# Performance work log

Measured on AMD Instinct MI355X. Metric: run time of the kernel, lower is better.

The kernel has to match this reference:

```python
import jax, jax.numpy as jnp
import numpy as np

N_USER, N_REST, D, E, Q = 200000, 50000, 64, 2000000, 500000


def setup_inputs() -> dict:
    key = jax.random.key(0)
    ks = jax.random.split(key, 16)
    s = 0.05
    return {
        "x_user": jax.random.normal(ks[0], (N_USER, D), jnp.float32),
        "x_rest": jax.random.normal(ks[1], (N_REST, D), jnp.float32),
        "Wl": jax.random.normal(ks[2], (3, 2, D, D), jnp.float32) * s,
        "Wr": jax.random.normal(ks[3], (3, 2, D, D), jnp.float32) * s,
        "bl": jnp.zeros((3, 2, D), jnp.float32),
        "dW1": jax.random.normal(ks[4], (D, 2 * D), jnp.float32) * s,
        "db1": jnp.zeros((D,), jnp.float32),
        "dW2": jax.random.normal(ks[5], (D, D), jnp.float32) * s,
        "db2": jnp.zeros((D,), jnp.float32),
        "dW3": jax.random.normal(ks[6], (1, D), jnp.float32) * s,
        "db3": jnp.zeros((1,), jnp.float32),
        "ur_src": jax.random.randint(ks[7], (E,), 0, N_USER, jnp.int32),
        "ur_dst": jax.random.randint(ks[8], (E,), 0, N_REST, jnp.int32),
        "ru_src": jax.random.randint(ks[9], (E,), 0, N_REST, jnp.int32),
        "ru_dst": jax.random.randint(ks[10], (E,), 0, N_USER, jnp.int32),
        "el_row": jax.random.randint(ks[11], (Q,), 0, N_USER, jnp.int32),
        "el_col": jax.random.randint(ks[12], (Q,), 0, N_REST, jnp.int32),
    }


def _sage(h_src, h_dst, src, dst, W_l, b_l, W_r):
    # PyG SAGEConv: lin_l(mean_{j in N(i)} x_j) + lin_r(x_i); bias on lin_l only.
    n_dst = h_dst.shape[0]
    agg = jax.ops.segment_sum(h_src[src], dst, num_segments=n_dst)  # [n_dst, D]
    cnt = jax.ops.segment_sum(jnp.ones_like(dst, dtype=h_src.dtype), dst, num_segments=n_dst)
    mean = agg / jnp.maximum(cnt, 1)[:, None]
    return mean @ W_l.T + b_l + h_dst @ W_r.T


def reference(x_user, x_rest, Wl, Wr, bl, dW1, db1, dW2, db2, dW3, db3,
              ur_src, ur_dst, ru_src, ru_dst, el_row, el_col):
    hu, hr = x_user, x_rest
    for l in range(3):
        # edge type 0: user -> restaurant ('rates'); edge type 1: reverse
        zr = _sage(hu, hr, ur_src, ur_dst, Wl[l, 0], bl[l, 0], Wr[l, 0])
        zu = _sage(hr, hu, ru_src, ru_dst, Wl[l, 1], bl[l, 1], Wr[l, 1])
        if l < 2:
            zr, zu = jax.nn.relu(zr), jax.nn.relu(zu)
        hu, hr = zu, zr
    # EdgeDecoder
    z = jnp.concatenate([hu[el_row], hr[el_col]], axis=-1)  # [Q, 2D]
    z = jax.nn.relu(z @ dW1.T + db1)
    z = jax.nn.relu(z @ dW2.T + db2)
    z = z @ dW3.T + db3
    return z.reshape(-1)
```

## Files before the change

### kernel.cpp

```cpp
#include <hip/hip_runtime.h>

#define NU 200000
#define NR 50000
#define DD 64
#define NE 2000000
#define NQ 500000
#define NBR 196
#define NBU 782
#define LDW 68

#define NBS 98
#define BKT_CAP 24576
#define LW_U 11
#define LW_R 9
#define PB_E 4096
#define NPBB 489

__global__ __launch_bounds__(256)
void binpass_kernel(const int* __restrict__ ru_src, const int* __restrict__ ru_dst,
                    const int* __restrict__ ur_src, const int* __restrict__ ur_dst,
                    int* __restrict__ bcur, int2* __restrict__ pairs) {
    __shared__ int2 stg[PB_E];
    __shared__ unsigned char gstg[PB_E];
    __shared__ int hist[256];
    __shared__ int sca[256], scb[256];
    __shared__ int gpos[128];
    int side = (blockIdx.x >= NPBB) ? 1 : 0;
    int blk = side ? (blockIdx.x - NPBB) : blockIdx.x;
    const int* src = side ? ur_src : ru_src;
    const int* dst = side ? ur_dst : ru_dst;
    int lw = side ? LW_R : LW_U;
    int* bc = bcur + side * NBS;
    int2* region = pairs + (size_t)side * NBS * BKT_CAP;
    int tid = threadIdx.x;
    hist[tid] = 0;
    __syncthreads();
    int base = blk * PB_E;
    int myg[16]; int myrank[16]; int2 myp[16];
#pragma unroll
    for (int i = 0; i < 16; i++) {
        int e = base + i * 256 + tid;
        if (e < NE) {
            int d = dst[e];
            int g = d >> lw;
            myg[i] = g;
            myp[i] = make_int2(src[e], d);
            myrank[i] = atomicAdd(&hist[g], 1);
        } else myg[i] = -1;
    }
    __syncthreads();
    int h = hist[tid];
    sca[tid] = h;
    __syncthreads();
    int* cur = sca; int* alt = scb;
    for (int off = 1; off < 256; off <<= 1) {
        int x = cur[tid];
        if (tid >= off) x += cur[tid - off];
        alt[tid] = x;
        __syncthreads();
        int* tmp = cur; cur = alt; alt = tmp;
    }
    alt[tid] = cur[tid] - h;
    if (tid < NBS && h > 0) gpos[tid] = atomicAdd(&bc[tid], h);
    __syncthreads();
    int* basep = alt;
#pragma unroll
    for (int i = 0; i < 16; i++) {
        if (myg[i] >= 0) {
            int p = basep[myg[i]] + myrank[i];
            stg[p] = myp[i];
            gstg[p] = (unsigned char)myg[i];
        }
    }
    __syncthreads();
    int tot = cur[255];
    for (int i = tid; i < tot; i += 256) {
        int g = gstg[i];
        int o = g * BKT_CAP + gpos[g] + (i - basep[g]);
        region[o] = stg[i];
    }
}

__global__ void bbase_kernel(const int* __restrict__ bcur, int* __restrict__ bbase,
                             int* __restrict__ rs_u, int* __restrict__ rs_r) {
    __shared__ int a[128], b[128];
    int sidx = blockIdx.x;
    const int* bc = bcur + sidx * NBS;
    int* bb = bbase + sidx * NBS;
    int tid = threadIdx.x;
    a[tid] = (tid < NBS) ? bc[tid] : 0;
    __syncthreads();
    int* cur = a; int* alt = b;
    for (int off = 1; off < 128; off <<= 1) {
        int t = cur[tid];
        if (tid >= off) t += cur[tid - off];
        alt[tid] = t;
        __syncthreads();
        int* tmp = cur; cur = alt; alt = tmp;
    }
    if (tid < NBS) bb[tid] = (tid == 0) ? 0 : cur[tid - 1];
    if (tid == 0) { if (sidx == 0) rs_u[NU] = NE; else rs_r[NR] = NE; }
}

__global__ __launch_bounds__(256)
void fillpass_kernel(const int2* __restrict__ pairs, const int* __restrict__ bcur,
                     const int* __restrict__ bbase,
                     int* __restrict__ rs_u, int* __restrict__ rs_r,
                     int* __restrict__ csr_u, int* __restrict__ csr_r) {
    __shared__ int win[BKT_CAP];
    __shared__ int lcnt[2048];
    __shared__ int lofs[2048];
    __shared__ int tsc[256], tsc2[256];
    int side = (blockIdx.x >= NBS) ? 1 : 0;
    int bkt = side ? (blockIdx.x - NBS) : blockIdx.x;
    const int2* reg = pairs + ((size_t)side * NBS + bkt) * BKT_CAP;
    int* rs = side ? rs_r : rs_u;
    int* csr = side ? csr_r : csr_u;
    int W = side ? 512 : 2048;
    int lw = side ? LW_R : LW_U;
    int n = side ? NR : NU;
    int d0 = bkt << lw;
    int tot = bcur[side * NBS + bkt];
    int base = bbase[side * NBS + bkt];
    int tid = threadIdx.x;
    for (int i = tid; i < W; i += 256) lcnt[i] = 0;
    __syncthreads();
    for (int i = tid; i < tot; i += 256) {
        int2 p = reg[i];
        atomicAdd(&lcnt[p.y - d0], 1);
    }
    __syncthreads();
    int per = W >> 8;
    int b0 = tid * per;
    int run = 0;
    for (int i = 0; i < per; i++) { int v = lcnt[b0 + i]; lofs[b0 + i] = run; run += v; }
    tsc[tid] = run;
    __syncthreads();
    int* cur = tsc; int* alt = tsc2;
    for (int off = 1; off < 256; off <<= 1) {
        int x = cur[tid];
        if (tid >= off) x += cur[tid - off];
        alt[tid] = x;
        __syncthreads();
        int* tmp = cur; cur = alt; alt = tmp;
    }
    int texcl = cur[tid] - run;
    for (int i = 0; i < per; i++) lofs[b0 + i] += texcl;
    __syncthreads();
    int wn = min(W, n - d0);
    for (int i = tid; i < wn; i += 256) rs[d0 + i] = base + lofs[i];
    __syncthreads();
    for (int i = tid; i < tot; i += 256) {
        int2 p = reg[i];
        int slot = atomicAdd(&lofs[p.y - d0], 1);
        win[slot] = p.x;
    }
    __syncthreads();
    for (int i = tid; i < tot; i += 256) csr[base + i] = win[i];
}

__global__ __launch_bounds__(256)
void gather2_kernel(const float* __restrict__ hu, const int* __restrict__ csr_r,
                    const int* __restrict__ rs_r, float* __restrict__ mean_r,
                    const float* __restrict__ hr, const int* __restrict__ csr_u,
                    const int* __restrict__ rs_u, float* __restrict__ mean_u) {
    int lane = threadIdx.x & 63;
    int wave = blockIdx.x * 4 + (threadIdx.x >> 6);
    const float* h; const int* csr; const int* rs; float* mean; int r;
    if (wave < NR) { h = hu; csr = csr_r; rs = rs_r; mean = mean_r; r = wave; }
    else if (wave < NR + NU) { h = hr; csr = csr_u; rs = rs_u; mean = mean_u; r = wave - NR; }
    else return;
    int s = rs[r], e = rs[r + 1];
    int g = lane >> 4;
    int fo = (lane & 15) << 2;
    float4 a0 = {0.f, 0.f, 0.f, 0.f};
    float4 a1 = {0.f, 0.f, 0.f, 0.f};
    for (int j = s; j < e; j += 64) {
        int rem = e - j;
        int nch = rem < 64 ? rem : 64;
        int li = lane < nch ? lane : nch - 1;
        int idx = csr[j + li];
        for (int kk = 0; kk < nch; kk += 8) {
            int j0 = kk + g;
            int j1 = kk + 4 + g;
            int i0 = __shfl(idx, j0);
            int i1 = __shfl(idx, j1);
            float4 x0 = *(const float4*)(h + (size_t)i0 * DD + fo);
            float4 x1 = *(const float4*)(h + (size_t)i1 * DD + fo);
            if (j0 < nch) { a0.x += x0.x; a0.y += x0.y; a0.z += x0.z; a0.w += x0.w; }
            if (j1 < nch) { a1.x += x1.x; a1.y += x1.y; a1.z += x1.z; a1.w += x1.w; }
        }
    }
    float4 acc;
    acc.x = a0.x + a1.x; acc.y = a0.y + a1.y;
    acc.z = a0.z + a1.z; acc.w = a0.w + a1.w;
    acc.x += __shfl_xor(acc.x, 16); acc.y += __shfl_xor(acc.y, 16);
    acc.z += __shfl_xor(acc.z, 16); acc.w += __shfl_xor(acc.w, 16);
    acc.x += __shfl_xor(acc.x, 32); acc.y += __shfl_xor(acc.y, 32);
    acc.z += __shfl_xor(acc.z, 32); acc.w += __shfl_xor(acc.w, 32);
    if (g == 0) {
        float inv = 1.0f / fmaxf((float)(e - s), 1.0f);
        acc.x *= inv; acc.y *= inv; acc.z *= inv; acc.w *= inv;
        *(float4*)(mean + (size_t)r * DD + fo) = acc;
    }
}

#define DOT4(A, B) ((A).x*(B).x + (A).y*(B).y + (A).z*(B).z + (A).w*(B).w)

__global__ __launch_bounds__(256, 2)
void sage_fused_kernel(const float* __restrict__ mean_r, const float* __restrict__ hr,
                       const float* __restrict__ mean_u, const float* __restrict__ hu,
                       const float* __restrict__ Wl2, const float* __restrict__ Wr2,
                       const float* __restrict__ bl2,
                       float* __restrict__ out_r, float* __restrict__ out_u, int do_relu) {
    __shared__ __attribute__((aligned(16))) float Wls[DD * LDW];
    __shared__ __attribute__((aligned(16))) float Wrs[DD * LDW];
    __shared__ __attribute__((aligned(16))) float Ms[64 * LDW];
    __shared__ __attribute__((aligned(16))) float Xs[64 * LDW];
    __shared__ float bsh[DD];
    int side = (blockIdx.x < NBR) ? 0 : 1;
    const float* Wl = Wl2 + side * DD * DD;
    const float* Wr = Wr2 + side * DD * DD;
    const float* bl = bl2 + side * DD;
    const float* mean; const float* h; float* out; int n; int blk;
    if (side == 0) { mean = mean_r; h = hr; out = out_r; n = NR; blk = blockIdx.x; }
    else { mean = mean_u; h = hu; out = out_u; n = NU; blk = blockIdx.x - NBR; }
    int tid = threadIdx.x;
    for (int i = tid; i < DD * DD; i += 256) {
        int c = i >> 6, k = i & 63;
        Wls[c * LDW + k] = Wl[i];
        Wrs[c * LDW + k] = Wr[i];
    }
    if (tid < DD) bsh[tid] = bl[tid];
    int rgrp = tid & 15;
    int cgrp = tid >> 4;
    int cb = cgrp * 4;
    int r00 = blk * 256;
    for (int ch = 0; ch < 4; ch++) {
        int rc0 = r00 + ch * 64;
        __syncthreads();
        for (int i = tid; i < 1024; i += 256) {
            int row = i >> 4;
            int c4 = (i & 15) << 2;
            int gr = min(rc0 + row, n - 1);
            *(float4*)&Ms[row * LDW + c4] = *(const float4*)(mean + (size_t)gr * DD + c4);
            *(float4*)&Xs[row * LDW + c4] = *(const float4*)(h + (size_t)gr * DD + c4);
        }
        __syncthreads();
        float4 bias = {bsh[cb], bsh[cb + 1], bsh[cb + 2], bsh[cb + 3]};
        float4 acc0 = bias, acc1 = bias, acc2 = bias, acc3 = bias;
#pragma unroll 1
        for (int kc = 0; kc < DD; kc += 8) {
            float4 wl[4][2], wr[4][2];
#pragma unroll
            for (int c = 0; c < 4; c++) {
                wl[c][0] = *(const float4*)&Wls[(cb + c) * LDW + kc];
                wl[c][1] = *(const float4*)&Wls[(cb + c) * LDW + kc + 4];
                wr[c][0] = *(const float4*)&Wrs[(cb + c) * LDW + kc];
                wr[c][1] = *(const float4*)&Wrs[(cb + c) * LDW + kc + 4];
            }
#define SROW(J, ACC) { \
            int row_ = rgrp + 16 * (J); \
            float4 ma_ = *(const float4*)&Ms[row_ * LDW + kc]; \
            float4 mb_ = *(const float4*)&Ms[row_ * LDW + kc + 4]; \
            float4 xa_ = *(const float4*)&Xs[row_ * LDW + kc]; \
            float4 xb_ = *(const float4*)&Xs[row_ * LDW + kc + 4]; \
            ACC.x += DOT4(ma_,wl[0][0])+DOT4(mb_,wl[0][1])+DOT4(xa_,wr[0][0])+DOT4(xb_,wr[0][1]); \
            ACC.y += DOT4(ma_,wl[1][0])+DOT4(mb_,wl[1][1])+DOT4(xa_,wr[1][0])+DOT4(xb_,wr[1][1]); \
            ACC.z += DOT4(ma_,wl[2][0])+DOT4(mb_,wl[2][1])+DOT4(xa_,wr[2][0])+DOT4(xb_,wr[2][1]); \
            ACC.w += DOT4(ma_,wl[3][0])+DOT4(mb_,wl[3][1])+DOT4(xa_,wr[3][0])+DOT4(xb_,wr[3][1]); }
            SROW(0, acc0) SROW(1, acc1) SROW(2, acc2) SROW(3, acc3)
#undef SROW
        }
        if (do_relu) {
            acc0.x = fmaxf(acc0.x, 0.f); acc0.y = fmaxf(acc0.y, 0.f); acc0.z = fmaxf(acc0.z, 0.f); acc0.w = fmaxf(acc0.w, 0.f);
            acc1.x = fmaxf(acc1.x, 0.f); acc1.y = fmaxf(acc1.y, 0.f); acc1.z = fmaxf(acc1.z, 0.f); acc1.w = fmaxf(acc1.w, 0.f);
            acc2.x = fmaxf(acc2.x, 0.f); acc2.y = fmaxf(acc2.y, 0.f); acc2.z = fmaxf(acc2.z, 0.f); acc2.w = fmaxf(acc2.w, 0.f);
            acc3.x = fmaxf(acc3.x, 0.f); acc3.y = fmaxf(acc3.y, 0.f); acc3.z = fmaxf(acc3.z, 0.f); acc3.w = fmaxf(acc3.w, 0.f);
        }
        {
            int r0_ = rc0 + rgrp;
            if (r0_ < n)      *(float4*)(out + (size_t)r0_ * DD + cb) = acc0;
            if (r0_ + 16 < n) *(float4*)(out + (size_t)(r0_ + 16) * DD + cb) = acc1;
            if (r0_ + 32 < n) *(float4*)(out + (size_t)(r0_ + 32) * DD + cb) = acc2;
            if (r0_ + 48 < n) *(float4*)(out + (size_t)(r0_ + 48) * DD + cb) = acc3;
        }
    }
}

__global__ __launch_bounds__(256, 2)
void pre_fused_kernel(const float* __restrict__ hu, const float* __restrict__ hr,
                      const float* __restrict__ dW1, const float* __restrict__ db1,
                      float* __restrict__ P_u, float* __restrict__ P_r) {
    __shared__ __attribute__((aligned(16))) float Ws[DD * LDW];
    __shared__ __attribute__((aligned(16))) float Xs[64 * LDW];
    __shared__ float bsh[DD];
    int side = (blockIdx.x < NBU) ? 0 : 1;
    int koff = side ? DD : 0;
    const float* h; float* out; int n; int blk;
    if (side == 0) { h = hu; out = P_u; n = NU; blk = blockIdx.x; }
    else { h = hr; out = P_r; n = NR; blk = blockIdx.x - NBU; }
    int tid = threadIdx.x;
    for (int i = tid; i < DD * DD; i += 256) {
        int c = i >> 6, k = i & 63;
        Ws[c * LDW + k] = dW1[c * 2 * DD + koff + k];
    }
    if (tid < DD) bsh[tid] = side ? 0.f : db1[tid];
    int rgrp = tid & 15;
    int cgrp = tid >> 4;
    int cb = cgrp * 4;
    int r00 = blk * 256;
    for (int ch = 0; ch < 4; ch++) {
        int rc0 = r00 + ch * 64;
        __syncthreads();
        for (int i = tid; i < 1024; i += 256) {
            int row = i >> 4;
            int c4 = (i & 15) << 2;
            int gr = min(rc0 + row, n - 1);
            *(float4*)&Xs[row * LDW + c4] = *(const float4*)(h + (size_t)gr * DD + c4);
        }
        __syncthreads();
        float4 bias = {bsh[cb], bsh[cb + 1], bsh[cb + 2], bsh[cb + 3]};
        float4 acc0 = bias, acc1 = bias, acc2 = bias, acc3 = bias;
#pragma unroll 1
        for (int kc = 0; kc < DD; kc += 8) {
            float4 wv[4][2];
#pragma unroll
            for (int c = 0; c < 4; c++) {
                wv[c][0] = *(const float4*)&Ws[(cb + c) * LDW + kc];
                wv[c][1] = *(const float4*)&Ws[(cb + c) * LDW + kc + 4];
            }
#define PROW(J, ACC) { \
            int row_ = rgrp + 16 * (J); \
            float4 xa_ = *(const float4*)&Xs[row_ * LDW + kc]; \
            float4 xb_ = *(const float4*)&Xs[row_ * LDW + kc + 4]; \
            ACC.x += DOT4(xa_,wv[0][0])+DOT4(xb_,wv[0][1]); \
            ACC.y += DOT4(xa_,wv[1][0])+DOT4(xb_,wv[1][1]); \
            ACC.z += DOT4(xa_,wv[2][0])+DOT4(xb_,wv[2][1]); \
            ACC.w += DOT4(xa_,wv[3][0])+DOT4(xb_,wv[3][1]); }
            PROW(0, acc0) PROW(1, acc1) PROW(2, acc2) PROW(3, acc3)
#undef PROW
        }
        {
            int r0_ = rc0 + rgrp;
            if (r0_ < n)      *(float4*)(out + (size_t)r0_ * DD + cb) = acc0;
            if (r0_ + 16 < n) *(float4*)(out + (size_t)(r0_ + 16) * DD + cb) = acc1;
            if (r0_ + 32 < n) *(float4*)(out + (size_t)(r0_ + 32) * DD + cb) = acc2;
            if (r0_ + 48 < n) *(float4*)(out + (size_t)(r0_ + 48) * DD + cb) = acc3;
        }
    }
}

#define ZCOMB(Zi, i) float4 Zi; { float4 u_ = pu[i]; float4 v_ = pr[i]; \
    Zi.x = fmaxf(u_.x + v_.x, 0.f); Zi.y = fmaxf(u_.y + v_.y, 0.f); \
    Zi.z = fmaxf(u_.z + v_.z, 0.f); Zi.w = fmaxf(u_.w + v_.w, 0.f); }

__global__ __launch_bounds__(256, 2)
void decoder_kernel(const float* __restrict__ Pu, const float* __restrict__ Pr,
                    const int* __restrict__ el_row, const int* __restrict__ el_col,
                    const float* __restrict__ dW2, const float* __restrict__ db2,
                    const float* __restrict__ dW3, const float* __restrict__ db3,
                    float* __restrict__ out) {
    __shared__ float W2s[DD * DD];
    __shared__ float b2s[DD], w3s[DD];
    for (int i = threadIdx.x; i < DD * DD; i += 256) W2s[i] = dW2[i];
    if (threadIdx.x < DD) {
        b2s[threadIdx.x] = db2[threadIdx.x];
        w3s[threadIdx.x] = dW3[threadIdx.x];
    }
    __syncthreads();
    int q = blockIdx.x * 256 + threadIdx.x;
    if (q >= NQ) return;
    int row = el_row[q], col = el_col[q];
    const float4* pu = (const float4*)(Pu + (size_t)row * DD);
    const float4* pr = (const float4*)(Pr + (size_t)col * DD);
    ZCOMB(z0, 0)  ZCOMB(z1, 1)  ZCOMB(z2, 2)  ZCOMB(z3, 3)
    ZCOMB(z4, 4)  ZCOMB(z5, 5)  ZCOMB(z6, 6)  ZCOMB(z7, 7)
    ZCOMB(z8, 8)  ZCOMB(z9, 9)  ZCOMB(z10, 10) ZCOMB(z11, 11)
    ZCOMB(z12, 12) ZCOMB(z13, 13) ZCOMB(z14, 14) ZCOMB(z15, 15)
    float o = db3[0];
#pragma unroll 2
    for (int c = 0; c < DD; c++) {
        const float4* wp = (const float4*)(W2s + c * DD);
        float s = b2s[c]
            + DOT4(z0, wp[0])  + DOT4(z1, wp[1])  + DOT4(z2, wp[2])  + DOT4(z3, wp[3])
            + DOT4(z4, wp[4])  + DOT4(z5, wp[5])  + DOT4(z6, wp[6])  + DOT4(z7, wp[7])
            + DOT4(z8, wp[8])  + DOT4(z9, wp[9])  + DOT4(z10, wp[10]) + DOT4(z11, wp[11])
            + DOT4(z12, wp[12]) + DOT4(z13, wp[13]) + DOT4(z14, wp[14]) + DOT4(z15, wp[15]);
        o += fmaxf(s, 0.f) * w3s[c];
    }
    out[q] = o;
}

extern "C" void kernel_launch(void* const* d_in, const int* in_sizes, int n_in,
                              void* d_out, int out_size, void* d_ws, size_t ws_size,
                              hipStream_t stream) {
    const float* x_user = (const float*)d_in[0];
    const float* x_rest = (const float*)d_in[1];
    const float* Wl     = (const float*)d_in[2];
    const float* Wr     = (const float*)d_in[3];
    const float* bl     = (const float*)d_in[4];
    const float* dW1    = (const float*)d_in[5];
    const float* db1    = (const float*)d_in[6];
    const float* dW2    = (const float*)d_in[7];
    const float* db2    = (const float*)d_in[8];
    const float* dW3    = (const float*)d_in[9];
    const float* db3    = (const float*)d_in[10];
    const int* ur_src   = (const int*)d_in[11];
    const int* ur_dst   = (const int*)d_in[12];
    const int* ru_src   = (const int*)d_in[13];
    const int* ru_dst   = (const int*)d_in[14];
    const int* el_row   = (const int*)d_in[15];
    const int* el_col   = (const int*)d_in[16];
    float* out = (float*)d_out;

    char* w = (char*)d_ws;
    size_t off = 0;
    auto alloc = [&](size_t bytes) -> void* {
        void* p = (void*)(w + off);
        off += (bytes + 255) & ~(size_t)255;
        return p;
    };
    float* hu0    = (float*)alloc((size_t)NU * DD * 4);
    float* hu1    = (float*)alloc((size_t)NU * DD * 4);
    float* hr0    = (float*)alloc((size_t)NR * DD * 4);
    float* hr1    = (float*)alloc((size_t)NR * DD * 4);
    float* mean_u = (float*)alloc((size_t)NU * DD * 4);
    float* mean_r = (float*)alloc((size_t)NR * DD * 4);
    int* csr_u  = (int*)alloc((size_t)NE * 4);
    int* csr_r  = (int*)alloc((size_t)NE * 4);
    int* rs_u   = (int*)alloc((size_t)(NU + 1) * 4);
    int* rs_r   = (int*)alloc((size_t)(NR + 1) * 4);
    int* bcur   = (int*)alloc((size_t)2 * NBS * 4);
    int* bbase  = (int*)alloc((size_t)2 * NBS * 4);

    int2* pairs = (int2*)mean_u;

    hipMemsetAsync(bcur, 0, (size_t)2 * NBS * 4, stream);
    binpass_kernel<<<2 * NPBB, 256, 0, stream>>>(ru_src, ru_dst, ur_src, ur_dst,
                                                 bcur, pairs);
    bbase_kernel<<<2, 128, 0, stream>>>(bcur, bbase, rs_u, rs_r);
    fillpass_kernel<<<2 * NBS, 256, 0, stream>>>(pairs, bcur, bbase,
                                                 rs_u, rs_r, csr_u, csr_r);

    const float* cu = x_user;
    const float* cr = x_rest;
    float* nu_[3] = {hu0, hu1, hu0};
    float* nr_[3] = {hr0, hr1, hr0};
    const int ggrid = (NR + NU + 3) / 4;

    for (int l = 0; l < 3; l++) {
        const float* Wl2 = Wl + (size_t)l * 2 * DD * DD;
        const float* Wr2 = Wr + (size_t)l * 2 * DD * DD;
        const float* bl2 = bl + (size_t)l * 2 * DD;
        int relu = (l < 2) ? 1 : 0;
        gather2_kernel<<<ggrid, 256, 0, stream>>>(cu, csr_r, rs_r, mean_r,
                                                  cr, csr_u, rs_u, mean_u);
        sage_fused_kernel<<<NBR + NBU, 256, 0, stream>>>(mean_r, cr, mean_u, cu,
                                                         Wl2, Wr2, bl2,
                                                         nr_[l], nu_[l], relu);
        cu = nu_[l];
        cr = nr_[l];
    }
    float* P_u = hu1;
    float* P_r = hr1;
    pre_fused_kernel<<<NBU + NBR, 256, 0, stream>>>(cu, cr, dW1, db1, P_u, P_r);
    decoder_kernel<<<(NQ + 255) / 256, 256, 0, stream>>>(P_u, P_r, el_row, el_col,
                                                         dW2, db2, dW3, db3, out);
}
```

Measured before the change: 1.001 ms.

## Bin decoder queries by user-row window and stage user rows in LDS

Measured after the change: 1.165 ms. 1.16x slower.

```diff
diff --git a/kernel.cpp b/kernel.cpp
--- a/kernel.cpp
+++ b/kernel.cpp
@@ -15,6 +15,12 @@
 #define LW_R 9
 #define PB_E 4096
 #define NPBB 489
+
+#define QWIN 448
+#define NQW 447
+#define QCAP 1536
+#define QB_E 4096
+#define NQB 123
 
 __global__ __launch_bounds__(256)
 void binpass_kernel(const int* __restrict__ ru_src, const int* __restrict__ ru_dst,
@@ -351,45 +357,133 @@
     }
 }
 
-#define ZCOMB(Zi, i) float4 Zi; { float4 u_ = pu[i]; float4 v_ = pr[i]; \
-    Zi.x = fmaxf(u_.x + v_.x, 0.f); Zi.y = fmaxf(u_.y + v_.y, 0.f); \
-    Zi.z = fmaxf(u_.z + v_.z, 0.f); Zi.w = fmaxf(u_.w + v_.w, 0.f); }
-
-__global__ __launch_bounds__(256, 2)
-void decoder_kernel(const float* __restrict__ Pu, const float* __restrict__ Pr,
-                    const int* __restrict__ el_row, const int* __restrict__ el_col,
-                    const float* __restrict__ dW2, const float* __restrict__ db2,
-                    const float* __restrict__ dW3, const float* __restrict__ db3,
-                    float* __restrict__ out) {
-    __shared__ float W2s[DD * DD];
-    __shared__ float b2s[DD], w3s[DD];
-    for (int i = threadIdx.x; i < DD * DD; i += 256) W2s[i] = dW2[i];
-    if (threadIdx.x < DD) {
-        b2s[threadIdx.x] = db2[threadIdx.x];
-        w3s[threadIdx.x] = dW3[threadIdx.x];
-    }
-    __syncthreads();
-    int q = blockIdx.x * 256 + threadIdx.x;
-    if (q >= NQ) return;
-    int row = el_row[q], col = el_col[q];
-    const float4* pu = (const float4*)(Pu + (size_t)row * DD);
-    const float4* pr = (const float4*)(Pr + (size_t)col * DD);
-    ZCOMB(z0, 0)  ZCOMB(z1, 1)  ZCOMB(z2, 2)  ZCOMB(z3, 3)
-    ZCOMB(z4, 4)  ZCOMB(z5, 5)  ZCOMB(z6, 6)  ZCOMB(z7, 7)
-    ZCOMB(z8, 8)  ZCOMB(z9, 9)  ZCOMB(z10, 10) ZCOMB(z11, 11)
-    ZCOMB(z12, 12) ZCOMB(z13, 13) ZCOMB(z14, 14) ZCOMB(z15, 15)
-    float o = db3[0];
-#pragma unroll 2
-    for (int c = 0; c < DD; c++) {
-        const float4* wp = (const float4*)(W2s + c * DD);
-        float s = b2s[c]
-            + DOT4(z0, wp[0])  + DOT4(z1, wp[1])  + DOT4(z2, wp[2])  + DOT4(z3, wp[3])
-            + DOT4(z4, wp[4])  + DOT4(z5, wp[5])  + DOT4(z6, wp[6])  + DOT4(z7, wp[7])
-            + DOT4(z8, wp[8])  + DOT4(z9, wp[9])  + DOT4(z10, wp[10]) + DOT4(z11, wp[11])
-            + DOT4(z12, wp[12]) + DOT4(z13, wp[13]) + DOT4(z14, wp[14]) + DOT4(z15, wp[15]);
-        o += fmaxf(s, 0.f) * w3s[c];
-    }
-    out[q] = o;
+__global__ __launch_bounds__(256)
+void qbin_kernel(const int* __restrict__ el_row, const int* __restrict__ el_col,
+                 int* __restrict__ qcur, int2* __restrict__ qpairs) {
+    __shared__ int2 stg[QB_E];
+    __shared__ unsigned short gstg[QB_E];
+    __shared__ int hist[512];
+    __shared__ int sca[256], scb[256];
+    __shared__ int gbase[512];
+    __shared__ int gpos[512];
+    int tid = threadIdx.x;
+    hist[tid] = 0; hist[tid + 256] = 0;
+    __syncthreads();
+    int base = blockIdx.x * QB_E;
+    int myg[16]; int myrank[16]; int2 myp[16];
+#pragma unroll
+    for (int i = 0; i < 16; i++) {
+        int e = base + i * 256 + tid;
+        if (e < NQ) {
+            int row = el_row[e];
+            int col = el_col[e];
+            int g = row / QWIN;
+            int rowl = row - g * QWIN;
+            myg[i] = g;
+            myp[i] = make_int2((rowl << 16) | col, e);
+            myrank[i] = atomicAdd(&hist[g], 1);
+        } else myg[i] = -1;
+    }
+    __syncthreads();
+    int b0 = tid * 2;
+    int h0 = hist[b0], h1 = hist[b0 + 1];
+    int run = h0 + h1;
+    sca[tid] = run;
+    __syncthreads();
+    int* cur = sca; int* alt = scb;
+    for (int off = 1; off < 256; off <<= 1) {
+        int x = cur[tid];
+        if (tid >= off) x += cur[tid - off];
+        alt[tid] = x;
+        __syncthreads();
+        int* tmp = cur; cur = alt; alt = tmp;
+    }
+    int texcl = cur[tid] - run;
+    gbase[b0] = texcl;
+    gbase[b0 + 1] = texcl + h0;
+    if (b0 < NQW && h0 > 0) gpos[b0] = atomicAdd(&qcur[b0], h0);
+    if (b0 + 1 < NQW && h1 > 0) gpos[b0 + 1] = atomicAdd(&qcur[b0 + 1], h1);
+    __syncthreads();
+#pragma unroll
+    for (int i = 0; i < 16; i++) {
+        if (myg[i] >= 0) {
+            int p = gbase[myg[i]] + myrank[i];
+            stg[p] = myp[i];
+            gstg[p] = (unsigned short)myg[i];
+        }
+    }
+    __syncthreads();
+    int tot = cur[255];
+    for (int i = tid; i < tot; i += 256) {
+        int g = gstg[i];
+        int o = g * QCAP + gpos[g] + (i - gbase[g]);
+        qpairs[o] = stg[i];
+    }
+}
+
+__device__ __forceinline__ float rdlane(float v, int l) {
+    return __int_as_float(__builtin_amdgcn_readlane(__float_as_int(v), l));
+}
+
+__global__ __launch_bounds__(512)
+void qdec_kernel(const float* __restrict__ Pu, const float* __restrict__ Pr,
+                 const int2* __restrict__ qpairs, const int* __restrict__ qcur,
+                 const float* __restrict__ dW2, const float* __restrict__ db2,
+                 const float* __restrict__ dW3, const float* __restrict__ db3,
+                 float* __restrict__ out) {
+    __shared__ __attribute__((aligned(16))) float Pus[QWIN * 68];
+    int w = blockIdx.x;
+    int tid = threadIdx.x;
+    int lane = tid & 63;
+    int wv = tid >> 6;
+    int r0 = w * QWIN;
+    for (int i = tid; i < QWIN * 16; i += 512) {
+        int row = i >> 4, c4 = (i & 15) << 2;
+        int gr = min(r0 + row, NU - 1);
+        *(float4*)&Pus[row * 68 + c4] = *(const float4*)(Pu + (size_t)gr * DD + c4);
+    }
+    float w2[64];
+    {
+        const float* wr = dW2 + (size_t)lane * DD;
+#pragma unroll
+        for (int k = 0; k < 64; k += 4) {
+            float4 v = *(const float4*)(wr + k);
+            w2[k] = v.x; w2[k + 1] = v.y; w2[k + 2] = v.z; w2[k + 3] = v.w;
+        }
+    }
+    float b2l = db2[lane];
+    float w3l = dW3[lane];
+    float db3v = db3[0];
+    __syncthreads();
+    int tot = qcur[w];
+    const int2* qp = qpairs + (size_t)w * QCAP;
+    for (int qi = wv; qi < tot; qi += 16) {
+        int2 pA = qp[qi];
+        int hasB = (qi + 8) < tot;
+        int2 pB = qp[hasB ? qi + 8 : qi];
+        float prA = Pr[(size_t)(pA.x & 0xFFFF) * DD + lane];
+        float prB = Pr[(size_t)(pB.x & 0xFFFF) * DD + lane];
+        float zA = fmaxf(Pus[(pA.x >> 16) * 68 + lane] + prA, 0.f);
+        float zB = fmaxf(Pus[(pB.x >> 16) * 68 + lane] + prB, 0.f);
+        float sA = b2l, sB = b2l;
+#pragma unroll
+        for (int k = 0; k < 64; k++) {
+            sA += rdlane(zA, k) * w2[k];
+            sB += rdlane(zB, k) * w2[k];
+        }
+        float tA = fmaxf(sA, 0.f) * w3l;
+        float tB = fmaxf(sB, 0.f) * w3l;
+        tA += __shfl_xor(tA, 1);  tB += __shfl_xor(tB, 1);
+        tA += __shfl_xor(tA, 2);  tB += __shfl_xor(tB, 2);
+        tA += __shfl_xor(tA, 4);  tB += __shfl_xor(tB, 4);
+        tA += __shfl_xor(tA, 8);  tB += __shfl_xor(tB, 8);
+        tA += __shfl_xor(tA, 16); tB += __shfl_xor(tB, 16);
+        tA += __shfl_xor(tA, 32); tB += __shfl_xor(tB, 32);
+        if (lane == 0) {
+            out[pA.y] = tA + db3v;
+            if (hasB) out[pB.y] = tB + db3v;
+        }
+    }
 }
 
 extern "C" void kernel_launch(void* const* d_in, const int* in_sizes, int n_in,
@@ -433,10 +527,12 @@
     int* rs_r   = (int*)alloc((size_t)(NR + 1) * 4);
     int* bcur   = (int*)alloc((size_t)2 * NBS * 4);
     int* bbase  = (int*)alloc((size_t)2 * NBS * 4);
+    int* qcur   = (int*)alloc((size_t)512 * 4);
 
     int2* pairs = (int2*)mean_u;
-
-    hipMemsetAsync(bcur, 0, (size_t)2 * NBS * 4, stream);
+    int2* qpairs = (int2*)mean_u;
+
+    hipMemsetAsync(bcur, 0, 4096, stream);
     binpass_kernel<<<2 * NPBB, 256, 0, stream>>>(ru_src, ru_dst, ur_src, ur_dst,
                                                  bcur, pairs);
     bbase_kernel<<<2, 128, 0, stream>>>(bcur, bbase, rs_u, rs_r);
@@ -465,6 +561,7 @@
     float* P_u = hu1;
     float* P_r = hr1;
     pre_fused_kernel<<<NBU + NBR, 256, 0, stream>>>(cu, cr, dW1, db1, P_u, P_r);
-    decoder_kernel<<<(NQ + 255) / 256, 256, 0, stream>>>(P_u, P_r, el_row, el_col,
-                                                         dW2, db2, dW3, db3, out);
-}
+    qbin_kernel<<<NQB, 256, 0, stream>>>(el_row, el_col, qcur, qpairs);
+    qdec_kernel<<<NQW, 512, 0, stream>>>(P_u, P_r, qpairs, qcur,
+                                         dW2, db2, dW3, db3, out);
+}
```
